# Kernel optimization log

Hardware: AMD Instinct MI355X
Metric: run time of the kernel (lower is better)

The kernel has to match this reference:

```python
import jax, jax.numpy as jnp
import numpy as np

B, N, IN_DIM, HID = 64, 1024, 128, 32


def _xavier(key, shape):
    # xavier_uniform_ on torch Linear weight [out, in]; we store [in, out]
    fan_in, fan_out = shape[0], shape[1]
    limit = float(np.sqrt(6.0 / (fan_in + fan_out)))
    return jax.random.uniform(key, shape, jnp.float32, -limit, limit)


def setup_inputs() -> dict:
    key = jax.random.key(0)
    ks = jax.random.split(key, 8)
    x = jax.random.normal(ks[0], (B, N, IN_DIM), jnp.float32)
    adj = jax.random.uniform(ks[1], (B, N, N), jnp.float32)  # dense adjacency
    W1 = _xavier(ks[2], (IN_DIM, HID))
    W2 = _xavier(ks[3], (HID, HID))
    W3 = _xavier(ks[4], (HID, HID))
    W4 = _xavier(ks[5], (HID, HID))
    b1 = jnp.zeros((HID,), jnp.float32)
    b2 = jnp.zeros((HID,), jnp.float32)
    b3 = jnp.zeros((HID,), jnp.float32)
    b4 = jnp.zeros((HID,), jnp.float32)
    a1 = jnp.float32(0.25)  # PReLU default init
    a2 = jnp.float32(0.25)
    a3 = jnp.float32(0.25)
    a4 = jnp.float32(0.25)
    return {"x": x, "adj": adj, "W1": W1, "W2": W2, "W3": W3, "W4": W4,
            "b1": b1, "b2": b2, "b3": b3, "b4": b4,
            "a1": a1, "a2": a2, "a3": a3, "a4": a4}


def _gcn_layer(x, adj, W, b, a):
    h = jnp.einsum('bnf,fo->bno', x, W)      # linear, no bias
    h = jnp.matmul(adj, h) + b               # aggregation + bias
    return jnp.where(h >= 0, h, a * h)       # PReLU


def reference(x, adj, W1, W2, W3, W4, b1, b2, b3, b4, a1, a2, a3, a4):
    h1 = _gcn_layer(x, adj, W1, b1, a1)
    h2 = _gcn_layer(h1, adj, W2, b2, a2)
    h3 = _gcn_layer(h2, adj, W3, b3, a3)
    h4 = _gcn_layer(h3, adj, W4, b4, a4)
    # sum-pool nodes per layer, concat along feature dim -> [B, 4*HID]
    return jnp.concatenate([h1.sum(axis=1), h2.sum(axis=1),
                            h3.sum(axis=1), h4.sum(axis=1)], axis=1)
```

## Files before the change

### kernel.cpp

```cpp
#include <hip/hip_runtime.h>
#include <hip/hip_bf16.h>

#define B_   64
#define N_   1024
#define IND_ 128
#define HID_ 32

typedef __attribute__((ext_vector_type(8))) short short8;
typedef __attribute__((ext_vector_type(4))) float f32x4;
typedef __attribute__((ext_vector_type(4))) unsigned int u32x4;
typedef unsigned short u16;

static __device__ __forceinline__ u16 f2bf(float f) {
    union { float f; unsigned int u; } v; v.f = f;
    unsigned int r = v.u + 0x7FFFu + ((v.u >> 16) & 1u);
    return (u16)(r >> 16);
}

template<int F>
__global__ __launch_bounds__(256) void linear_kernel(
    const float* __restrict__ in,
    const float* __restrict__ W,
    u16* __restrict__ outT)
{
    __shared__ float sW[F][HID_];
    const int tid = threadIdx.x;
    for (int e = tid; e < F * HID_; e += 256) sW[e / HID_][e % HID_] = W[e];
    __syncthreads();

    const int b = blockIdx.x >> 2;
    const int n = ((blockIdx.x & 3) << 8) + tid;
    const f32x4* row4 = (const f32x4*)(in + ((size_t)b * N_ + n) * F);

    float acc[HID_];
#pragma unroll
    for (int o = 0; o < HID_; ++o) acc[o] = 0.f;

#pragma unroll 4
    for (int f4 = 0; f4 < F / 4; ++f4) {
        f32x4 xv = row4[f4];
#pragma unroll
        for (int j = 0; j < 4; ++j) {
#pragma unroll
            for (int o = 0; o < HID_; ++o) acc[o] += xv[j] * sW[f4 * 4 + j][o];
        }
    }
    u16* op = outT + (size_t)b * HID_ * N_ + n;
#pragma unroll
    for (int o = 0; o < HID_; ++o) op[o * N_] = f2bf(acc[o]);
}

template<int MODE>
__global__ __launch_bounds__(256) void agg_kernel(
    const float* __restrict__ adjf,
    const u16*  __restrict__ adjb_in,
    u16*        __restrict__ adjb_out,
    const u16*  __restrict__ hlinT,
    float*      __restrict__ h,
    float*      __restrict__ partial,
    const float* __restrict__ bias,
    const float* __restrict__ alpha_p)
{
    __shared__ u16 sB[HID_][N_ + 8];
    __shared__ float pool[4][HID_];
    const int tid = threadIdx.x;
    const int b = blockIdx.y;

    {
        const u32x4* src = (const u32x4*)(hlinT + (size_t)b * HID_ * N_);
        for (int i = tid; i < (HID_ * N_) / 8; i += 256) {
            int c = (i * 8) >> 10;
            int k = (i * 8) & (N_ - 1);
            *(u32x4*)&sB[c][k] = src[i];
        }
    }
    __syncthreads();

    const int wid = tid >> 6, lane = tid & 63;
    const int r16 = lane & 15, g = lane >> 4;
    const int koff = g * 8;
    const int rowbase = blockIdx.x * 128 + wid * 32;
    const int row0 = rowbase + r16;
    const int row1 = row0 + 16;
    const size_t adj_b = (size_t)b * N_ * N_;

    f32x4 acc[2][2] = {};

    for (int k0 = 0; k0 < N_; k0 += 32) {
        short8 a0, a1;
        if (MODE == 0) {
            a0 = *(const short8*)&adjb_in[adj_b + (size_t)row0 * N_ + k0 + koff];
            a1 = *(const short8*)&adjb_in[adj_b + (size_t)row1 * N_ + k0 + koff];
        } else {
            const float* p0 = adjf + adj_b + (size_t)row0 * N_ + k0 + koff;
            const float* p1 = adjf + adj_b + (size_t)row1 * N_ + k0 + koff;
            f32x4 v00 = *(const f32x4*)p0, v01 = *(const f32x4*)(p0 + 4);
            f32x4 v10 = *(const f32x4*)p1, v11 = *(const f32x4*)(p1 + 4);
#pragma unroll
            for (int i = 0; i < 4; ++i) {
                a0[i]     = (short)f2bf(v00[i]);
                a0[i + 4] = (short)f2bf(v01[i]);
                a1[i]     = (short)f2bf(v10[i]);
                a1[i + 4] = (short)f2bf(v11[i]);
            }
            if (MODE == 1) {
                *(short8*)&adjb_out[adj_b + (size_t)row0 * N_ + k0 + koff] = a0;
                *(short8*)&adjb_out[adj_b + (size_t)row1 * N_ + k0 + koff] = a1;
            }
        }
        short8 b0 = *(const short8*)&sB[r16][k0 + koff];
        short8 b1 = *(const short8*)&sB[16 + r16][k0 + koff];
        acc[0][0] = __builtin_amdgcn_mfma_f32_16x16x32_bf16(a0, b0, acc[0][0], 0, 0, 0);
        acc[0][1] = __builtin_amdgcn_mfma_f32_16x16x32_bf16(a0, b1, acc[0][1], 0, 0, 0);
        acc[1][0] = __builtin_amdgcn_mfma_f32_16x16x32_bf16(a1, b0, acc[1][0], 0, 0, 0);
        acc[1][1] = __builtin_amdgcn_mfma_f32_16x16x32_bf16(a1, b1, acc[1][1], 0, 0, 0);
    }

    const float alpha = *alpha_p;
#pragma unroll
    for (int ct = 0; ct < 2; ++ct) {
        const int col = ct * 16 + r16;
        const float bv = bias[col];
        float ps = 0.f;
#pragma unroll
        for (int rt = 0; rt < 2; ++rt) {
#pragma unroll
            for (int r = 0; r < 4; ++r) {
                const int row = rowbase + rt * 16 + g * 4 + r;
                float v = acc[rt][ct][r] + bv;
                v = (v >= 0.f) ? v : alpha * v;
                h[((size_t)b * N_ + row) * HID_ + col] = v;
                ps += v;
            }
        }
        ps += __shfl_xor(ps, 16, 64);
        ps += __shfl_xor(ps, 32, 64);
        if (lane < 16) pool[wid][col] = ps;
    }
    __syncthreads();
    if (tid < HID_) {
        float s = pool[0][tid] + pool[1][tid] + pool[2][tid] + pool[3][tid];
        partial[((size_t)b * 8 + blockIdx.x) * HID_ + tid] = s;
    }
}

__global__ __launch_bounds__(256) void finalize_kernel(
    const float* __restrict__ partial,
    float* __restrict__ out)
{
    const int i = blockIdx.x * 256 + threadIdx.x;
    if (i >= B_ * 4 * HID_) return;
    const int b = i >> 7;
    const int rem = i & 127;
    const int l = rem >> 5;
    const int o = rem & 31;
    const float* p = partial + (((size_t)l * B_ + b) * 8) * HID_ + o;
    float s = 0.f;
#pragma unroll
    for (int t = 0; t < 8; ++t) s += p[t * HID_];
    out[i] = s;
}

extern "C" void kernel_launch(void* const* d_in, const int* in_sizes, int n_in,
                              void* d_out, int out_size, void* d_ws, size_t ws_size,
                              hipStream_t stream) {
    const float* x   = (const float*)d_in[0];
    const float* adj = (const float*)d_in[1];
    const float* W[4]  = {(const float*)d_in[2], (const float*)d_in[3],
                          (const float*)d_in[4], (const float*)d_in[5]};
    const float* bi[4] = {(const float*)d_in[6], (const float*)d_in[7],
                          (const float*)d_in[8], (const float*)d_in[9]};
    const float* al[4] = {(const float*)d_in[10], (const float*)d_in[11],
                          (const float*)d_in[12], (const float*)d_in[13]};
    float* out = (float*)d_out;

    const size_t adjb_bytes = (size_t)B_ * N_ * N_ * 2;
    const size_t hlin_bytes = (size_t)B_ * HID_ * N_ * 2;
    const size_t h_bytes    = (size_t)B_ * N_ * HID_ * 4;
    const size_t part_bytes = (size_t)4 * B_ * 8 * HID_ * 4;
    const bool full = ws_size >= adjb_bytes + hlin_bytes + h_bytes + part_bytes;

    char* p = (char*)d_ws;
    u16* adjb = nullptr;
    if (full) { adjb = (u16*)p; p += adjb_bytes; }
    u16*   hlinT   = (u16*)p;  p += hlin_bytes;
    float* h       = (float*)p; p += h_bytes;
    float* partial = (float*)p;

    const dim3 ga(8, 64);
    const int part_stride = B_ * 8 * HID_;

    linear_kernel<IND_><<<256, 256, 0, stream>>>(x, W[0], hlinT);
    if (full)
        agg_kernel<1><<<ga, 256, 0, stream>>>(adj, nullptr, adjb, hlinT, h,
                                              partial + 0, bi[0], al[0]);
    else
        agg_kernel<2><<<ga, 256, 0, stream>>>(adj, nullptr, nullptr, hlinT, h,
                                              partial + 0, bi[0], al[0]);
    for (int l = 1; l < 4; ++l) {
        linear_kernel<HID_><<<256, 256, 0, stream>>>(h, W[l], hlinT);
        if (full)
            agg_kernel<0><<<ga, 256, 0, stream>>>(nullptr, adjb, nullptr, hlinT, h,
                                                  partial + (size_t)l * part_stride,
                                                  bi[l], al[l]);
        else
            agg_kernel<2><<<ga, 256, 0, stream>>>(adj, nullptr, nullptr, hlinT, h,
                                                  partial + (size_t)l * part_stride,
                                                  bi[l], al[l]);
    }
    finalize_kernel<<<32, 256, 0, stream>>>(partial, out);
}
```

Baseline: 247.6 us.

## Fuse next layer's linear transform into aggregation epilogue and use nontemporal adj loads

In the full-workspace path, the aggregation kernel now writes its PReLU output tile to shared memory (unioned with the B buffer) and multiplies it by the next layer's weight. The result is emitted directly as the bf16 transposed hlin buffer for the next layer, ping-ponging between two buffers. This removes three separate linear kernel launches and the fp32 h round-trip through global memory. It also switches the fp32 adjacency reads in the first pass to nontemporal loads, which avoids cache pollution. The cost is an extra barrier, more shared memory, and a small per-block scalar matmul in the epilogue.

Result: faster. 222.3 us (-10.2%).

```diff
diff --git a/kernel.cpp b/kernel.cpp
--- a/kernel.cpp
+++ b/kernel.cpp
@@ -50,28 +50,39 @@
     for (int o = 0; o < HID_; ++o) op[o * N_] = f2bf(acc[o]);
 }
 
-template<int MODE>
+union AggSmem {
+    u16   sB[HID_][N_ + 8];
+    float h_s[128][33];
+};
+
+template<int MODE, int FUSE>
 __global__ __launch_bounds__(256) void agg_kernel(
     const float* __restrict__ adjf,
     const u16*  __restrict__ adjb_in,
     u16*        __restrict__ adjb_out,
-    const u16*  __restrict__ hlinT,
+    const u16*  __restrict__ hlinT_in,
+    u16*        __restrict__ hlinT_out,
+    const float* __restrict__ Wnext,
     float*      __restrict__ h,
     float*      __restrict__ partial,
     const float* __restrict__ bias,
     const float* __restrict__ alpha_p)
 {
-    __shared__ u16 sB[HID_][N_ + 8];
+    __shared__ AggSmem sm;
     __shared__ float pool[4][HID_];
+    __shared__ float sW2[HID_][HID_];
     const int tid = threadIdx.x;
     const int b = blockIdx.y;
 
+    if (FUSE) {
+        for (int e = tid; e < HID_ * HID_; e += 256) sW2[e >> 5][e & 31] = Wnext[e];
+    }
     {
-        const u32x4* src = (const u32x4*)(hlinT + (size_t)b * HID_ * N_);
+        const u32x4* src = (const u32x4*)(hlinT_in + (size_t)b * HID_ * N_);
         for (int i = tid; i < (HID_ * N_) / 8; i += 256) {
             int c = (i * 8) >> 10;
             int k = (i * 8) & (N_ - 1);
-            *(u32x4*)&sB[c][k] = src[i];
+            *(u32x4*)&sm.sB[c][k] = src[i];
         }
     }
     __syncthreads();
@@ -92,10 +103,12 @@
             a0 = *(const short8*)&adjb_in[adj_b + (size_t)row0 * N_ + k0 + koff];
             a1 = *(const short8*)&adjb_in[adj_b + (size_t)row1 * N_ + k0 + koff];
         } else {
-            const float* p0 = adjf + adj_b + (size_t)row0 * N_ + k0 + koff;
-            const float* p1 = adjf + adj_b + (size_t)row1 * N_ + k0 + koff;
-            f32x4 v00 = *(const f32x4*)p0, v01 = *(const f32x4*)(p0 + 4);
-            f32x4 v10 = *(const f32x4*)p1, v11 = *(const f32x4*)(p1 + 4);
+            const f32x4* p0 = (const f32x4*)(adjf + adj_b + (size_t)row0 * N_ + k0 + koff);
+            const f32x4* p1 = (const f32x4*)(adjf + adj_b + (size_t)row1 * N_ + k0 + koff);
+            f32x4 v00 = __builtin_nontemporal_load(p0);
+            f32x4 v01 = __builtin_nontemporal_load(p0 + 1);
+            f32x4 v10 = __builtin_nontemporal_load(p1);
+            f32x4 v11 = __builtin_nontemporal_load(p1 + 1);
 #pragma unroll
             for (int i = 0; i < 4; ++i) {
                 a0[i]     = (short)f2bf(v00[i]);
@@ -108,8 +121,8 @@
                 *(short8*)&adjb_out[adj_b + (size_t)row1 * N_ + k0 + koff] = a1;
             }
         }
-        short8 b0 = *(const short8*)&sB[r16][k0 + koff];
-        short8 b1 = *(const short8*)&sB[16 + r16][k0 + koff];
+        short8 b0 = *(const short8*)&sm.sB[r16][k0 + koff];
+        short8 b1 = *(const short8*)&sm.sB[16 + r16][k0 + koff];
         acc[0][0] = __builtin_amdgcn_mfma_f32_16x16x32_bf16(a0, b0, acc[0][0], 0, 0, 0);
         acc[0][1] = __builtin_amdgcn_mfma_f32_16x16x32_bf16(a0, b1, acc[0][1], 0, 0, 0);
         acc[1][0] = __builtin_amdgcn_mfma_f32_16x16x32_bf16(a1, b0, acc[1][0], 0, 0, 0);
@@ -117,30 +130,72 @@
     }
 
     const float alpha = *alpha_p;
+    float v[2][2][4];
+    float ps[2];
+#pragma unroll
+    for (int ct = 0; ct < 2; ++ct) {
+        const float bv = bias[ct * 16 + r16];
+        ps[ct] = 0.f;
+#pragma unroll
+        for (int rt = 0; rt < 2; ++rt) {
+#pragma unroll
+            for (int r = 0; r < 4; ++r) {
+                float x = acc[rt][ct][r] + bv;
+                x = (x >= 0.f) ? x : alpha * x;
+                v[ct][rt][r] = x;
+                ps[ct] += x;
+            }
+        }
+    }
+    __syncthreads();
+
 #pragma unroll
     for (int ct = 0; ct < 2; ++ct) {
         const int col = ct * 16 + r16;
-        const float bv = bias[col];
-        float ps = 0.f;
-#pragma unroll
-        for (int rt = 0; rt < 2; ++rt) {
-#pragma unroll
-            for (int r = 0; r < 4; ++r) {
-                const int row = rowbase + rt * 16 + g * 4 + r;
-                float v = acc[rt][ct][r] + bv;
-                v = (v >= 0.f) ? v : alpha * v;
-                h[((size_t)b * N_ + row) * HID_ + col] = v;
-                ps += v;
-            }
-        }
-        ps += __shfl_xor(ps, 16, 64);
-        ps += __shfl_xor(ps, 32, 64);
-        if (lane < 16) pool[wid][col] = ps;
-    }
-    __syncthreads();
+        float p = ps[ct];
+        p += __shfl_xor(p, 16, 64);
+        p += __shfl_xor(p, 32, 64);
+        if (lane < 16) pool[wid][col] = p;
+        if (FUSE) {
+#pragma unroll
+            for (int rt = 0; rt < 2; ++rt)
+#pragma unroll
+                for (int r = 0; r < 4; ++r)
+                    sm.h_s[wid * 32 + rt * 16 + g * 4 + r][col] = v[ct][rt][r];
+        }
+        if (MODE == 2) {
+#pragma unroll
+            for (int rt = 0; rt < 2; ++rt)
+#pragma unroll
+                for (int r = 0; r < 4; ++r) {
+                    const int row = rowbase + rt * 16 + g * 4 + r;
+                    h[((size_t)b * N_ + row) * HID_ + col] = v[ct][rt][r];
+                }
+        }
+    }
+    __syncthreads();
+
     if (tid < HID_) {
         float s = pool[0][tid] + pool[1][tid] + pool[2][tid] + pool[3][tid];
         partial[((size_t)b * 8 + blockIdx.x) * HID_ + tid] = s;
+    }
+
+    if (FUSE) {
+        const int r_local = tid >> 1;
+        const int obase = (tid & 1) * 16;
+        float acc2[16];
+#pragma unroll
+        for (int o = 0; o < 16; ++o) acc2[o] = 0.f;
+#pragma unroll 4
+        for (int k = 0; k < HID_; ++k) {
+            const float hv = sm.h_s[r_local][k];
+#pragma unroll
+            for (int o = 0; o < 16; ++o) acc2[o] += hv * sW2[k][obase + o];
+        }
+        const int n = blockIdx.x * 128 + r_local;
+        u16* op = hlinT_out + (size_t)b * HID_ * N_ + n;
+#pragma unroll
+        for (int o = 0; o < 16; ++o) op[(size_t)(obase + o) * N_] = f2bf(acc2[o]);
     }
 }
 
@@ -178,35 +233,52 @@
     const size_t hlin_bytes = (size_t)B_ * HID_ * N_ * 2;
     const size_t h_bytes    = (size_t)B_ * N_ * HID_ * 4;
     const size_t part_bytes = (size_t)4 * B_ * 8 * HID_ * 4;
-    const bool full = ws_size >= adjb_bytes + hlin_bytes + h_bytes + part_bytes;
-
-    char* p = (char*)d_ws;
-    u16* adjb = nullptr;
-    if (full) { adjb = (u16*)p; p += adjb_bytes; }
-    u16*   hlinT   = (u16*)p;  p += hlin_bytes;
-    float* h       = (float*)p; p += h_bytes;
-    float* partial = (float*)p;
+    const bool full = ws_size >= adjb_bytes + 2 * hlin_bytes + part_bytes;
 
     const dim3 ga(8, 64);
     const int part_stride = B_ * 8 * HID_;
 
-    linear_kernel<IND_><<<256, 256, 0, stream>>>(x, W[0], hlinT);
-    if (full)
-        agg_kernel<1><<<ga, 256, 0, stream>>>(adj, nullptr, adjb, hlinT, h,
-                                              partial + 0, bi[0], al[0]);
-    else
-        agg_kernel<2><<<ga, 256, 0, stream>>>(adj, nullptr, nullptr, hlinT, h,
-                                              partial + 0, bi[0], al[0]);
-    for (int l = 1; l < 4; ++l) {
-        linear_kernel<HID_><<<256, 256, 0, stream>>>(h, W[l], hlinT);
-        if (full)
-            agg_kernel<0><<<ga, 256, 0, stream>>>(nullptr, adjb, nullptr, hlinT, h,
-                                                  partial + (size_t)l * part_stride,
-                                                  bi[l], al[l]);
-        else
-            agg_kernel<2><<<ga, 256, 0, stream>>>(adj, nullptr, nullptr, hlinT, h,
-                                                  partial + (size_t)l * part_stride,
-                                                  bi[l], al[l]);
-    }
-    finalize_kernel<<<32, 256, 0, stream>>>(partial, out);
-}
+    if (full) {
+        char* p = (char*)d_ws;
+        u16* adjb  = (u16*)p;  p += adjb_bytes;
+        u16* hlinA = (u16*)p;  p += hlin_bytes;
+        u16* hlinB = (u16*)p;  p += hlin_bytes;
+        float* partial = (float*)p;
+
+        linear_kernel<IND_><<<256, 256, 0, stream>>>(x, W[0], hlinA);
+        agg_kernel<1, 1><<<ga, 256, 0, stream>>>(adj, nullptr, adjb, hlinA, hlinB,
+                                                 W[1], nullptr,
+                                                 partial + 0, bi[0], al[0]);
+        agg_kernel<0, 1><<<ga, 256, 0, stream>>>(nullptr, adjb, nullptr, hlinB, hlinA,
+                                                 W[2], nullptr,
+                                                 partial + (size_t)1 * part_stride,
+                                                 bi[1], al[1]);
+        agg_kernel<0, 1><<<ga, 256, 0, stream>>>(nullptr, adjb, nullptr, hlinA, hlinB,
+                                                 W[3], nullptr,
+                                                 partial + (size_t)2 * part_stride,
+                                                 bi[2], al[2]);
+        agg_kernel<0, 0><<<ga, 256, 0, stream>>>(nullptr, adjb, nullptr, hlinB, nullptr,
+                                                 nullptr, nullptr,
+                                                 partial + (size_t)3 * part_stride,
+                                                 bi[3], al[3]);
+    } else {
+        char* p = (char*)d_ws;
+        u16*   hlinT   = (u16*)p;  p += hlin_bytes;
+        float* h       = (float*)p; p += h_bytes;
+        float* partial = (float*)p;
+
+        linear_kernel<IND_><<<256, 256, 0, stream>>>(x, W[0], hlinT);
+        agg_kernel<2, 0><<<ga, 256, 0, stream>>>(adj, nullptr, nullptr, hlinT, nullptr,
+                                                 nullptr, h, partial + 0, bi[0], al[0]);
+        for (int l = 1; l < 4; ++l) {
+            linear_kernel<HID_><<<256, 256, 0, stream>>>(h, W[l], hlinT);
+            agg_kernel<2, 0><<<ga, 256, 0, stream>>>(adj, nullptr, nullptr, hlinT, nullptr,
+                                                     nullptr, h,
+                                                     partial + (size_t)l * part_stride,
+                                                     bi[l], al[l]);
+        }
+    }
+    finalize_kernel<<<32, 256, 0, stream>>>(
+        (const float*)((char*)d_ws + (full ? adjb_bytes + 2 * hlin_bytes
+                                           : hlin_bytes + h_bytes)), out);
+}
```
